# Optimization experiments

Measured on AMD Instinct MI355X. Metric: run time of the kernel, lower is better.

Reference implementation:

```python
import jax, jax.numpy as jnp
import numpy as np

N_NODES = 100000
N_EDGES = 1600000
C_IN, C_HID, C_OUT = 128, 128, 64


def setup_inputs() -> dict:
    key = jax.random.key(0)
    k1, k2, k3, k4, k5, k6 = jax.random.split(key, 6)
    x = jax.random.normal(k1, (N_NODES, C_IN), dtype=jnp.float32)
    edge_index = jax.random.randint(k2, (2, N_EDGES), 0, N_NODES, dtype=jnp.int64)
    # Glorot-style init for GCN weights, zero bias (PyG defaults)
    W1 = jax.random.normal(k3, (C_IN, C_HID), dtype=jnp.float32) * (1.0 / np.sqrt(C_IN))
    b1 = jnp.zeros((C_HID,), dtype=jnp.float32)
    W2 = jax.random.normal(k4, (C_HID, C_OUT), dtype=jnp.float32) * (1.0 / np.sqrt(C_HID))
    b2 = jnp.zeros((C_OUT,), dtype=jnp.float32)
    return {"x": x, "edge_index": edge_index, "W1": W1, "b1": b1, "W2": W2, "b2": b2}


def _gcn_conv(x, W, b, src, dst, norm, n_nodes):
    # x' = D^-1/2 (A + I) D^-1/2 (x W) + b   (PyG GCNConv default)
    h = x @ W                                  # [N, out]
    msg = h[src] * norm[:, None]               # gather + scale, [E', out]
    out = jax.ops.segment_sum(msg, dst, num_segments=n_nodes)  # scatter-add
    return out + b


def reference(x, edge_index, W1, b1, W2, b2):
    n = x.shape[0]
    loops = jnp.arange(n, dtype=edge_index.dtype)
    src = jnp.concatenate([edge_index[0], loops])  # self-loops appended
    dst = jnp.concatenate([edge_index[1], loops])
    # symmetric normalization: deg from destination index (incl. self-loops)
    deg = jax.ops.segment_sum(jnp.ones_like(dst, dtype=x.dtype), dst, num_segments=n)
    dis = jnp.where(deg > 0, jax.lax.rsqrt(deg), 0.0)
    norm = dis[src] * dis[dst]                 # [E + N]
    h = _gcn_conv(x, W1, b1, src, dst, norm, n)
    h = jax.nn.relu(h)                          # Dropout is identity at inference
    out = _gcn_conv(h, W2, b2, src, dst, norm, n)
    return out
```

## Files before the change

kernel.cpp:

```cpp
#include <hip/hip_runtime.h>

static constexpr int NPAD = 131072;
static constexpr int PAD = 48;
typedef unsigned int uint32;
typedef _Float16 f16;
typedef __attribute__((ext_vector_type(8))) _Float16 f16x8;
typedef __attribute__((ext_vector_type(4))) _Float16 f16x4;
typedef __attribute__((ext_vector_type(4))) float f32x4;

__device__ __forceinline__ ushort f2bf(float f) {
  uint32 u = __float_as_uint(f);
  return (ushort)((u + 0x7FFF + ((u >> 16) & 1)) >> 16);
}
__device__ __forceinline__ float bf_lo(uint32 u) { return __uint_as_float(u << 16); }
__device__ __forceinline__ float bf_hi(uint32 u) { return __uint_as_float(u & 0xFFFF0000u); }

__device__ __forceinline__ int lane_rank_in(unsigned long long mask) {
  return __builtin_amdgcn_mbcnt_hi((unsigned int)(mask >> 32),
                                   __builtin_amdgcn_mbcnt_lo((unsigned int)mask, 0));
}

__device__ __forceinline__ void bucket_body(const int* __restrict__ src,
                                            const int* __restrict__ dst,
                                            int* __restrict__ bcur,
                                            uint2* __restrict__ buckets,
                                            int* __restrict__ degi, int nN, int nE,
                                            unsigned long long magic, int bcap,
                                            int bb) {
  __shared__ int cnt[8];
  __shared__ int blkbase[8];
  const int t = threadIdx.x;
  {
    int z = bb * 256 + t;
    if (z < nN) degi[z] = 0;
  }
  if (t < 8) cnt[t] = 0;
  __syncthreads();
  const int e0 = bb * 2048;
  int sa[8], da[8], ba[8], off[8];
  bool va[8];
#pragma unroll
  for (int p = 0; p < 2; ++p) {
    int idx = e0 + p * 1024 + t * 4;
    if (idx + 4 <= nE) {
      int4 sv = *(const int4*)(src + idx);
      int4 dv = *(const int4*)(dst + idx);
      sa[p * 4 + 0] = sv.x; sa[p * 4 + 1] = sv.y; sa[p * 4 + 2] = sv.z; sa[p * 4 + 3] = sv.w;
      da[p * 4 + 0] = dv.x; da[p * 4 + 1] = dv.y; da[p * 4 + 2] = dv.z; da[p * 4 + 3] = dv.w;
      va[p * 4 + 0] = va[p * 4 + 1] = va[p * 4 + 2] = va[p * 4 + 3] = true;
    } else {
#pragma unroll
      for (int j = 0; j < 4; ++j) {
        int ii = idx + j;
        bool v = ii < nE;
        va[p * 4 + j] = v;
        sa[p * 4 + j] = v ? src[ii] : 0;
        da[p * 4 + j] = v ? dst[ii] : 0;
      }
    }
  }
#pragma unroll
  for (int j = 0; j < 8; ++j) {
    ba[j] = (int)(((unsigned long long)(uint32)da[j] * magic) >> 35);
    unsigned long long mv = __ballot(va[j]);
    unsigned long long m0 = __ballot((ba[j] & 1) != 0);
    unsigned long long m1 = __ballot((ba[j] & 2) != 0);
    unsigned long long m2 = __ballot((ba[j] & 4) != 0);
    unsigned long long meq = ((ba[j] & 1) ? m0 : ~m0) & ((ba[j] & 2) ? m1 : ~m1) &
                             ((ba[j] & 4) ? m2 : ~m2) & mv;
    if (va[j]) {
      int rank = lane_rank_in(meq);
      int tot = __popcll(meq);
      int leader = __ffsll(meq) - 1;
      int base = 0;
      if (rank == 0) base = atomicAdd(&cnt[ba[j]], tot);
      base = __shfl(base, leader, 64);
      off[j] = base + rank;
    } else {
      off[j] = 0;
    }
  }
  __syncthreads();
  if (t < 8) blkbase[t] = t * bcap + atomicAdd(&bcur[t], cnt[t]);
  __syncthreads();
#pragma unroll
  for (int j = 0; j < 8; ++j) {
    if (va[j]) buckets[blkbase[ba[j]] + off[j]] = make_uint2((uint32)sa[j], (uint32)da[j]);
  }
}

template <int COLS, bool RELU_IN>
__device__ __forceinline__ void gemm_mfma_body(const float* __restrict__ X,
                                               const float* __restrict__ W,
                                               ushort* __restrict__ H, int n,
                                               int bid) {
  constexpr int NS = COLS / 16;
  constexpr int LDK = 40;
  __shared__ f16 sAh[128][LDK];
  __shared__ f16 sAl[128][LDK];
  __shared__ f16 sBh[COLS][LDK];
  __shared__ f16 sBl[COLS][LDK];
  const int t = threadIdx.x;
  const int row0 = bid * 128;
  const int wv = t >> 6;
  const int l = t & 63;
  const int fr = l & 15;
  const int fkb = (l >> 4) * 8;

  f32x4 acc[2][NS];
#pragma unroll
  for (int m = 0; m < 2; ++m)
#pragma unroll
    for (int nt = 0; nt < NS; ++nt) acc[m][nt] = (f32x4){0.f, 0.f, 0.f, 0.f};

  for (int k0 = 0; k0 < 128; k0 += 32) {
#pragma unroll
    for (int p = 0; p < 4; ++p) {
      int idx = p * 256 + t;
      int r = idx >> 3;
      int f = idx & 7;
      int gr = row0 + r;
      float4 v = make_float4(0.f, 0.f, 0.f, 0.f);
      if (gr < n) v = *(const float4*)(X + (size_t)gr * 128 + k0 + f * 4);
      if (RELU_IN) {
        v.x = fmaxf(v.x, 0.f); v.y = fmaxf(v.y, 0.f);
        v.z = fmaxf(v.z, 0.f); v.w = fmaxf(v.w, 0.f);
      }
      f16x4 hv, lv;
      hv.x = (f16)v.x; lv.x = (f16)(v.x - (float)hv.x);
      hv.y = (f16)v.y; lv.y = (f16)(v.y - (float)hv.y);
      hv.z = (f16)v.z; lv.z = (f16)(v.z - (float)hv.z);
      hv.w = (f16)v.w; lv.w = (f16)(v.w - (float)hv.w);
      *(f16x4*)&sAh[r][f * 4] = hv;
      *(f16x4*)&sAl[r][f * 4] = lv;
    }
    constexpr int WP = (32 * COLS) / (256 * 4);
#pragma unroll
    for (int p = 0; p < WP; ++p) {
      int idx = p * 256 + t;
      int k = idx / (COLS / 4);
      int c4 = idx % (COLS / 4);
      float4 v = *(const float4*)(W + (size_t)(k0 + k) * COLS + c4 * 4);
      f16 hh;
      hh = (f16)v.x; sBh[c4 * 4 + 0][k] = hh; sBl[c4 * 4 + 0][k] = (f16)(v.x - (float)hh);
      hh = (f16)v.y; sBh[c4 * 4 + 1][k] = hh; sBl[c4 * 4 + 1][k] = (f16)(v.y - (float)hh);
      hh = (f16)v.z; sBh[c4 * 4 + 2][k] = hh; sBl[c4 * 4 + 2][k] = (f16)(v.z - (float)hh);
      hh = (f16)v.w; sBh[c4 * 4 + 3][k] = hh; sBl[c4 * 4 + 3][k] = (f16)(v.w - (float)hh);
    }
    __syncthreads();
    const f16x8 ah0 = *(const f16x8*)&sAh[wv * 32 + fr][fkb];
    const f16x8 ah1 = *(const f16x8*)&sAh[wv * 32 + 16 + fr][fkb];
    const f16x8 al0 = *(const f16x8*)&sAl[wv * 32 + fr][fkb];
    const f16x8 al1 = *(const f16x8*)&sAl[wv * 32 + 16 + fr][fkb];
#pragma unroll
    for (int nt = 0; nt < NS; ++nt) {
      const f16x8 bh = *(const f16x8*)&sBh[nt * 16 + fr][fkb];
      const f16x8 bl = *(const f16x8*)&sBl[nt * 16 + fr][fkb];
      acc[0][nt] = __builtin_amdgcn_mfma_f32_16x16x32_f16(ah0, bh, acc[0][nt], 0, 0, 0);
      acc[1][nt] = __builtin_amdgcn_mfma_f32_16x16x32_f16(ah1, bh, acc[1][nt], 0, 0, 0);
      acc[0][nt] = __builtin_amdgcn_mfma_f32_16x16x32_f16(al0, bh, acc[0][nt], 0, 0, 0);
      acc[1][nt] = __builtin_amdgcn_mfma_f32_16x16x32_f16(al1, bh, acc[1][nt], 0, 0, 0);
      acc[0][nt] = __builtin_amdgcn_mfma_f32_16x16x32_f16(ah0, bl, acc[0][nt], 0, 0, 0);
      acc[1][nt] = __builtin_amdgcn_mfma_f32_16x16x32_f16(ah1, bl, acc[1][nt], 0, 0, 0);
    }
    __syncthreads();
  }
#pragma unroll
  for (int m = 0; m < 2; ++m)
#pragma unroll
    for (int nt = 0; nt < NS; ++nt)
#pragma unroll
      for (int j = 0; j < 4; ++j) {
        int row = row0 + wv * 32 + m * 16 + (l >> 4) * 4 + j;
        if (row < n) H[(size_t)row * COLS + nt * 16 + fr] = f2bf(acc[m][nt][j]);
      }
}

__global__ __launch_bounds__(256) void gemm1_bucket_kernel(
    const float* __restrict__ X, const float* __restrict__ W,
    ushort* __restrict__ H, int n, const int* __restrict__ src,
    const int* __restrict__ dst, int* __restrict__ bcur,
    uint2* __restrict__ buckets, int* __restrict__ degi, int nE,
    unsigned long long magic, int bcap, int gemmBlocks) {
  const int b = (int)blockIdx.x;
  if (b < gemmBlocks) {
    gemm_mfma_body<128, false>(X, W, H, n, b);
  } else {
    bucket_body(src, dst, bcur, buckets, degi, n, nE, magic, bcap, b - gemmBlocks);
  }
}

__global__ __launch_bounds__(256) void gemm2_kernel(const float* __restrict__ X,
                                                    const float* __restrict__ W,
                                                    ushort* __restrict__ H, int n) {
  gemm_mfma_body<64, true>(X, W, H, n, (int)blockIdx.x);
}

__global__ __launch_bounds__(1024) void fillpad2_kernel(
    const uint2* __restrict__ buckets, const int* __restrict__ bcur,
    int* __restrict__ degi, int* __restrict__ csrp, int bcap, int nPerXcd,
    int nN, int npb) {
  __shared__ int cnt[512];
  const int t = threadIdx.x;
  const int xcd = (int)blockIdx.x & 7;
  const int sub = (int)blockIdx.x >> 3;
  const int lo = xcd * nPerXcd + sub * npb;
  const int hi = min(min(lo + npb, (xcd + 1) * nPerXcd), nN);
  if (lo >= hi) return;
  for (int k = t; k < npb; k += 1024) cnt[k] = 0;
  __syncthreads();
  const int cntb = bcur[xcd];
  const uint2* B = buckets + (size_t)xcd * bcap;
  int i = t * 8;
  for (; i + 7 < cntb; i += 8192) {
    uint4 p0 = *(const uint4*)&B[i];
    uint4 p1 = *(const uint4*)&B[i + 2];
    uint4 p2 = *(const uint4*)&B[i + 4];
    uint4 p3 = *(const uint4*)&B[i + 6];
    int s[8] = {(int)p0.x, (int)p0.z, (int)p1.x, (int)p1.z,
                (int)p2.x, (int)p2.z, (int)p3.x, (int)p3.z};
    int d[8] = {(int)p0.y, (int)p0.w, (int)p1.y, (int)p1.w,
                (int)p2.y, (int)p2.w, (int)p3.y, (int)p3.w};
#pragma unroll
    for (int k = 0; k < 8; ++k) {
      if (d[k] >= lo && d[k] < hi) {
        int pos = atomicAdd(&cnt[d[k] - lo], 1);
        if (pos < PAD) csrp[(size_t)d[k] * PAD + pos] = s[k];
      }
    }
  }
  {
    int jend = min(i + 8, cntb);
    for (int j = i; j < jend; ++j) {
      uint2 e = B[j];
      int dd = (int)e.y;
      if (dd >= lo && dd < hi) {
        int pos = atomicAdd(&cnt[dd - lo], 1);
        if (pos < PAD) csrp[(size_t)dd * PAD + pos] = (int)e.x;
      }
    }
  }
  __syncthreads();
  for (int k = t; k < hi - lo; k += 1024) degi[lo + k] = cnt[k];
}

template <int COLS>
__global__ __launch_bounds__(256) void agg_kernel(const int* __restrict__ degi,
                                                  const int* __restrict__ csrp,
                                                  const ushort* __restrict__ h,
                                                  const float* __restrict__ bias,
                                                  float* __restrict__ out, int n,
                                                  int nPerXcd) {
  __shared__ uint2 sE[4][64];
  const int t = threadIdx.x;
  const int lane = t & 63;
  const int wid = t >> 6;
  const int xcd = blockIdx.x & 7;
  const int sub = (int)blockIdx.x >> 3;
  const int nwv = (gridDim.x >> 3) * 4;
  const int d0 = xcd * nPerXcd;
  const int d1 = min(d0 + nPerXcd, n);
  float2 bv2 = make_float2(0.f, 0.f);
  float bv1 = 0.f;
  if (COLS == 128) bv2 = ((const float2*)bias)[lane];
  else bv1 = bias[lane];

  int d = d0 + sub * 4 + wid;
  if (d >= d1) return;

  int degA = min(degi[d], PAD);
  int sA = (lane < degA) ? csrp[(size_t)d * PAD + lane] : 0;
  float wA = (lane < degA) ? rsqrtf((float)degi[sA] + 1.0f) : 0.f;
  int dB = d + nwv;
  int degB = 0, sRawB = 0;
  if (dB < d1) {
    degB = degi[dB];
    if (lane < PAD) sRawB = csrp[(size_t)dB * PAD + lane];
  }

  while (true) {
    const float dd = rsqrtf((float)degA + 1.0f);
    const bool hasB = dB < d1;
    int sB = 0, gB = 0;
    if (hasB) {
      int dgc = min(degB, PAD);
      sB = (lane < dgc) ? sRawB : 0;
      gB = degi[sB];
    }
    const int dC = dB + nwv;
    int degC = 0, sRawC = 0;
    if (dC < d1) {
      degC = degi[dC];
      if (lane < PAD) sRawC = csrp[(size_t)dC * PAD + lane];
    }
    sE[wid][lane] = make_uint2((uint32)sA, __float_as_uint(wA));
    if (COLS == 128) {
      uint32 hv = ((const uint32*)(h + (size_t)d * 128))[lane];
      float acx = 0.f, acy = 0.f;
      for (int j0 = 0; j0 < degA; j0 += 8) {
        uint32 a[8];
        float w[8];
#pragma unroll
        for (int k = 0; k < 8; ++k) {
          uint2 e = sE[wid][j0 + k];
          w[k] = __uint_as_float(e.y);
          a[k] = ((const uint32*)(h + (size_t)e.x * 128))[lane];
        }
#pragma unroll
        for (int k = 0; k < 8; ++k) {
          acx = fmaf(w[k], bf_lo(a[k]), acx);
          acy = fmaf(w[k], bf_hi(a[k]), acy);
        }
      }
      float ox = fmaf(dd, fmaf(dd, bf_lo(hv), acx), bv2.x);
      float oy = fmaf(dd, fmaf(dd, bf_hi(hv), acy), bv2.y);
      ((float2*)(out + (size_t)d * 128))[lane] = make_float2(ox, oy);
    } else {
      uint32 hv = (uint32)h[(size_t)d * 64 + lane];
      float acc = 0.f;
      for (int j0 = 0; j0 < degA; j0 += 8) {
        uint32 a[8];
        float w[8];
#pragma unroll
        for (int k = 0; k < 8; ++k) {
          uint2 e = sE[wid][j0 + k];
          w[k] = __uint_as_float(e.y);
          a[k] = (uint32)h[(size_t)e.x * 64 + lane];
        }
#pragma unroll
        for (int k = 0; k < 8; ++k) acc = fmaf(w[k], bf_lo(a[k]), acc);
      }
      out[(size_t)d * 64 + lane] = fmaf(dd, fmaf(dd, bf_lo(hv), acc), bv1);
    }
    if (!hasB) break;
    const int dgc = min(degB, PAD);
    wA = (lane < dgc) ? rsqrtf((float)gB + 1.0f) : 0.f;
    sA = sB;
    degA = dgc;
    d = dB;
    dB = dC;
    degB = degC;
    sRawB = sRawC;
  }
}

extern "C" void kernel_launch(void* const* d_in, const int* in_sizes, int n_in,
                              void* d_out, int out_size, void* d_ws, size_t ws_size,
                              hipStream_t stream) {
  const float* x  = (const float*)d_in[0];
  const int* ei   = (const int*)d_in[1];
  const float* W1 = (const float*)d_in[2];
  const float* b1 = (const float*)d_in[3];
  const float* W2 = (const float*)d_in[4];
  const float* b2 = (const float*)d_in[5];
  float* out = (float*)d_out;

  const int N = in_sizes[0] / 128;
  const int E = in_sizes[1] / 2;
  const int* srcI = ei;
  const int* dstI = ei + E;
  const int nPerXcd = (N + 7) / 8;
  const unsigned long long magic =
      ((1ULL << 35) + (unsigned long long)nPerXcd - 1) / (unsigned long long)nPerXcd;

  char* w = (char*)d_ws;
  int* degi       = (int*)w;                   w += (size_t)NPAD * 4;
  int* bcur       = (int*)w;                   w += 64 * 4;
  int* csrp       = (int*)w;                   w += (size_t)(N + 64) * PAD * 4;
  ushort* h       = (ushort*)w;                w += (size_t)N * 128 * 2;
  float* out1     = (float*)w;
  ushort* g       = h;
  uint2* buckets  = (uint2*)out1;
  const int bcap = E / 8 + 16384;

  const int gemmBlocks = (N + 127) / 128;
  const int bucketBlocks = (E + 2047) / 2048;
  const int SUB = 32;
  const int npb = (nPerXcd + SUB - 1) / SUB;

  hipMemsetAsync(bcur, 0, 64 * sizeof(int), stream);
  gemm1_bucket_kernel<<<gemmBlocks + bucketBlocks, 256, 0, stream>>>(
      x, W1, h, N, srcI, dstI, bcur, buckets, degi, E, magic, bcap, gemmBlocks);
  fillpad2_kernel<<<8 * SUB, 1024, 0, stream>>>(buckets, bcur, degi, csrp, bcap,
                                                nPerXcd, N, npb);
  agg_kernel<128><<<2048, 256, 0, stream>>>(degi, csrp, h, b1, out1, N, nPerXcd);
  gemm2_kernel<<<gemmBlocks, 256, 0, stream>>>(out1, W2, g, N);
  agg_kernel<64><<<2048, 256, 0, stream>>>(degi, csrp, g, b2, out, N, nPerXcd);
}
```

Baseline: 304.0 us.

## Software-prefetch bucket loads in fillpad and double sub-partitions and agg grid

The fillpad kernel's bucket scan now loads the next 8-edge chunk into registers before processing the current one, hiding global load latency behind the shared-memory atomics. The sub-partition count per XCD doubles from 32 to 64, halving nodes per block so the shared counter array shrinks to 256. This gives more blocks, but each block rescans the whole XCD bucket, so total bucket read traffic doubles. Both aggregation launches also double their grid from 2048 to 4096 blocks.

```diff
diff --git a/kernel.cpp b/kernel.cpp
--- a/kernel.cpp
+++ b/kernel.cpp
@@ -200,7 +200,7 @@
     const uint2* __restrict__ buckets, const int* __restrict__ bcur,
     int* __restrict__ degi, int* __restrict__ csrp, int bcap, int nPerXcd,
     int nN, int npb) {
-  __shared__ int cnt[512];
+  __shared__ int cnt[256];
   const int t = threadIdx.x;
   const int xcd = (int)blockIdx.x & 7;
   const int sub = (int)blockIdx.x >> 3;
@@ -212,15 +212,24 @@
   const int cntb = bcur[xcd];
   const uint2* B = buckets + (size_t)xcd * bcap;
   int i = t * 8;
-  for (; i + 7 < cntb; i += 8192) {
-    uint4 p0 = *(const uint4*)&B[i];
-    uint4 p1 = *(const uint4*)&B[i + 2];
-    uint4 p2 = *(const uint4*)&B[i + 4];
-    uint4 p3 = *(const uint4*)&B[i + 6];
-    int s[8] = {(int)p0.x, (int)p0.z, (int)p1.x, (int)p1.z,
-                (int)p2.x, (int)p2.z, (int)p3.x, (int)p3.z};
-    int d[8] = {(int)p0.y, (int)p0.w, (int)p1.y, (int)p1.w,
-                (int)p2.y, (int)p2.w, (int)p3.y, (int)p3.w};
+  uint4 q0, q1, q2, q3;
+  bool have = (i + 7 < cntb);
+  if (have) {
+    q0 = *(const uint4*)&B[i];     q1 = *(const uint4*)&B[i + 2];
+    q2 = *(const uint4*)&B[i + 4]; q3 = *(const uint4*)&B[i + 6];
+  }
+  while (have) {
+    const int ni = i + 8192;
+    uint4 n0, n1, n2, n3;
+    const bool hnext = (ni + 7 < cntb);
+    if (hnext) {
+      n0 = *(const uint4*)&B[ni];     n1 = *(const uint4*)&B[ni + 2];
+      n2 = *(const uint4*)&B[ni + 4]; n3 = *(const uint4*)&B[ni + 6];
+    }
+    int s[8] = {(int)q0.x, (int)q0.z, (int)q1.x, (int)q1.z,
+                (int)q2.x, (int)q2.z, (int)q3.x, (int)q3.z};
+    int d[8] = {(int)q0.y, (int)q0.w, (int)q1.y, (int)q1.w,
+                (int)q2.y, (int)q2.w, (int)q3.y, (int)q3.w};
 #pragma unroll
     for (int k = 0; k < 8; ++k) {
       if (d[k] >= lo && d[k] < hi) {
@@ -228,6 +237,9 @@
         if (pos < PAD) csrp[(size_t)d[k] * PAD + pos] = s[k];
       }
     }
+    i = ni;
+    q0 = n0; q1 = n1; q2 = n2; q3 = n3;
+    have = hnext;
   }
   {
     int jend = min(i + 8, cntb);
@@ -375,7 +387,7 @@
 
   const int gemmBlocks = (N + 127) / 128;
   const int bucketBlocks = (E + 2047) / 2048;
-  const int SUB = 32;
+  const int SUB = 64;
   const int npb = (nPerXcd + SUB - 1) / SUB;
 
   hipMemsetAsync(bcur, 0, 64 * sizeof(int), stream);
@@ -383,7 +395,7 @@
       x, W1, h, N, srcI, dstI, bcur, buckets, degi, E, magic, bcap, gemmBlocks);
   fillpad2_kernel<<<8 * SUB, 1024, 0, stream>>>(buckets, bcur, degi, csrp, bcap,
                                                 nPerXcd, N, npb);
-  agg_kernel<128><<<2048, 256, 0, stream>>>(degi, csrp, h, b1, out1, N, nPerXcd);
+  agg_kernel<128><<<4096, 256, 0, stream>>>(degi, csrp, h, b1, out1, N, nPerXcd);
   gemm2_kernel<<<gemmBlocks, 256, 0, stream>>>(out1, W2, g, N);
-  agg_kernel<64><<<2048, 256, 0, stream>>>(degi, csrp, g, b2, out, N, nPerXcd);
-}
+  agg_kernel<64><<<4096, 256, 0, stream>>>(degi, csrp, g, b2, out, N, nPerXcd);
+}
```

New measurement: 325.3 us. 7.0% more time.
